# Kernel optimization log

Measured on AMD Instinct MI355X. Metric: run time of the kernel, lower is better.

The kernel has to match this reference:

```python
import jax, jax.numpy as jnp
import numpy as np

B, S, H, NH = 8, 512, 1024, 16
HD = H // NH          # 64
MAXP = 512            # max_position_embeddings


def setup_inputs() -> dict:
    key = jax.random.key(0)
    ks = jax.random.split(key, 6)
    sc = 0.02
    return {
        "hidden_states": jax.random.normal(ks[0], (B, S, H), jnp.float32),
        "attention_mask": jnp.zeros((B, 1, 1, S), jnp.float32),
        "Wq": jax.random.normal(ks[1], (H, H), jnp.float32) * sc,
        "bq": jnp.zeros((H,), jnp.float32),
        "Wk": jax.random.normal(ks[2], (H, H), jnp.float32) * sc,
        "bk": jnp.zeros((H,), jnp.float32),
        "Wv": jax.random.normal(ks[3], (H, H), jnp.float32) * sc,
        "bv": jnp.zeros((H,), jnp.float32),
        "dist_emb": jax.random.normal(ks[4], (2 * MAXP - 1, HD), jnp.float32) * sc,
    }


def reference(hidden_states, attention_mask, Wq, bq, Wk, bk, Wv, bv, dist_emb):
    b, s, h = hidden_states.shape
    nh, hd = NH, h // NH

    def heads(x):  # [b,s,h] -> [b,nh,s,hd]
        return x.reshape(b, s, nh, hd).transpose(0, 2, 1, 3)

    q = heads(hidden_states @ Wq.T + bq)
    k = heads(hidden_states @ Wk.T + bk)
    v = heads(hidden_states @ Wv.T + bv)

    # raw QK^T scores [b,nh,s,s]
    scores = jnp.einsum("bhld,bhrd->bhlr", q, k)

    # relative_key positional bias
    dist = jnp.arange(s)[:, None] - jnp.arange(s)[None, :] + (MAXP - 1)
    pos = dist_emb[dist]  # [s,s,hd]
    scores = scores + jnp.einsum("bhld,lrd->bhlr", q, pos)

    scores = scores / jnp.sqrt(jnp.asarray(hd, scores.dtype))
    scores = scores + attention_mask  # additive mask, broadcasts [b,1,1,s]

    probs = jax.nn.softmax(scores, axis=-1)  # dropout p=0 (eval)
    ctx = jnp.einsum("bhlr,bhrd->bhld", probs, v)
    ctx = ctx.transpose(0, 2, 1, 3).reshape(b, s, h)
    return ctx
```

## Files before the change

kernel.cpp:

```cpp
#include <hip/hip_runtime.h>

#define BB 8
#define SS 512
#define HH 1024
#define NHH 16
#define HDD 64

typedef short short8 __attribute__((ext_vector_type(8)));
typedef float f32x4 __attribute__((ext_vector_type(4)));
typedef unsigned short ushort;

union U4S8 { unsigned u[4]; short8 s; uint4 v; };

__device__ __forceinline__ void split2(float f0, float f1,
                                       unsigned& hi, unsigned& lo)
{
    unsigned u0 = __builtin_bit_cast(unsigned, f0);
    unsigned u1 = __builtin_bit_cast(unsigned, f1);
    hi = __builtin_amdgcn_perm(u1, u0, 0x07060302u);
    float r0 = f0 - __builtin_bit_cast(float, u0 & 0xffff0000u);
    float r1 = f1 - __builtin_bit_cast(float, u1 & 0xffff0000u);
    unsigned v0 = __builtin_bit_cast(unsigned, r0);
    unsigned v1 = __builtin_bit_cast(unsigned, r1);
    lo = __builtin_amdgcn_perm(v1, v0, 0x07060302u);
}

__device__ __forceinline__ unsigned pack_hi2(float f0, float f1) {
    return __builtin_amdgcn_perm(__builtin_bit_cast(unsigned, f1),
                                 __builtin_bit_cast(unsigned, f0), 0x07060302u);
}
__device__ __forceinline__ ushort bf16_rne(float f) {
    unsigned u = __builtin_bit_cast(unsigned, f);
    u += 0x7fffu + ((u >> 16) & 1u);
    return (ushort)(u >> 16);
}
__device__ __forceinline__ ushort bf16_tr(float f) {
    return (ushort)(__builtin_bit_cast(unsigned, f) >> 16);
}
__device__ __forceinline__ float bf16f(ushort s) {
    unsigned u = ((unsigned)s) << 16;
    return __builtin_bit_cast(float, u);
}
__device__ __forceinline__ int swel(int row, int col) {
    return row * 64 + ((((col >> 3) ^ (row & 7)) << 3) | (col & 7));
}

__global__ __launch_bounds__(256)
void qkv_proj_kernel(const float* __restrict__ HS,
                     const float* __restrict__ Wq, const float* __restrict__ bq,
                     const float* __restrict__ Wk, const float* __restrict__ bk,
                     const float* __restrict__ Wv, const float* __restrict__ bv,
                     ushort* __restrict__ Qh, ushort* __restrict__ Ql,
                     ushort* __restrict__ Kh, ushort* __restrict__ Kl,
                     ushort* __restrict__ Vh, ushort* __restrict__ Vl)
{
    const int bx = blockIdx.x;
    const int by = blockIdx.y;
    const int z   = bx >> 3;
    const int nf0 = (bx & 7) * 128;
    const int m0  = by * 128;

    const float* W    = (z == 0) ? Wq : (z == 1) ? Wk : Wv;
    const float* bias = (z == 0) ? bq : (z == 1) ? bk : bv;
    ushort* OutH = (z == 0) ? Qh : (z == 1) ? Kh : Vh;
    ushort* OutL = (z == 0) ? Ql : (z == 1) ? Kl : Vl;
    const float sc = (z == 0) ? 0.125f : 1.0f;

    __shared__ short Ah[128][32];
    __shared__ short Al[128][32];
    __shared__ short Bh[128][32];
    __shared__ short Bl[128][32];

    const int tid  = threadIdx.x;
    const int lane = tid & 63;
    const int wave = tid >> 6;
    const int wm   = (wave & 1) * 64;
    const int wn   = (wave >> 1) * 64;

    const int srow = tid >> 1;
    const int skh  = (tid & 1) * 16;

    const int fr    = lane & 15;
    const int kslot = lane >> 4;

    f32x4 acc[4][4];
#pragma unroll
    for (int i = 0; i < 4; i++)
#pragma unroll
        for (int j = 0; j < 4; j++) acc[i][j] = (f32x4)0.0f;

    for (int k0 = 0; k0 < HH; k0 += 32) {
        __syncthreads();
        {
            float ra[16], rb[16];
            const float* pa = HS + (size_t)(m0 + srow) * HH + k0 + skh;
            const float* pb = W + (size_t)(nf0 + srow) * HH + k0 + skh;
#pragma unroll
            for (int u = 0; u < 4; u++) {
                *(float4*)&ra[4 * u] = *(const float4*)(pa + 4 * u);
                *(float4*)&rb[4 * u] = *(const float4*)(pb + 4 * u);
            }
            unsigned ha[8], la[8], hb[8], lb[8];
#pragma unroll
            for (int p = 0; p < 8; p++) {
                split2(ra[2 * p], ra[2 * p + 1], ha[p], la[p]);
                split2(rb[2 * p], rb[2 * p + 1], hb[p], lb[p]);
            }
            *(uint4*)&Ah[srow][skh]     = *(uint4*)&ha[0];
            *(uint4*)&Ah[srow][skh + 8] = *(uint4*)&ha[4];
            *(uint4*)&Al[srow][skh]     = *(uint4*)&la[0];
            *(uint4*)&Al[srow][skh + 8] = *(uint4*)&la[4];
            *(uint4*)&Bh[srow][skh]     = *(uint4*)&hb[0];
            *(uint4*)&Bh[srow][skh + 8] = *(uint4*)&hb[4];
            *(uint4*)&Bl[srow][skh]     = *(uint4*)&lb[0];
            *(uint4*)&Bl[srow][skh + 8] = *(uint4*)&lb[4];
        }
        __syncthreads();

        short8 a_h[4], a_l[4], b_h[4], b_l[4];
#pragma unroll
        for (int i = 0; i < 4; i++) {
            a_h[i] = *(const short8*)&Ah[wm + i * 16 + fr][kslot * 8];
            a_l[i] = *(const short8*)&Al[wm + i * 16 + fr][kslot * 8];
            b_h[i] = *(const short8*)&Bh[wn + i * 16 + fr][kslot * 8];
            b_l[i] = *(const short8*)&Bl[wn + i * 16 + fr][kslot * 8];
        }
#pragma unroll
        for (int i = 0; i < 4; i++)
#pragma unroll
            for (int j = 0; j < 4; j++) {
                acc[i][j] = __builtin_amdgcn_mfma_f32_16x16x32_bf16(a_h[i], b_h[j], acc[i][j], 0, 0, 0);
                acc[i][j] = __builtin_amdgcn_mfma_f32_16x16x32_bf16(a_h[i], b_l[j], acc[i][j], 0, 0, 0);
                acc[i][j] = __builtin_amdgcn_mfma_f32_16x16x32_bf16(a_l[i], b_h[j], acc[i][j], 0, 0, 0);
            }
    }

    const int cn  = lane & 15;
    const int rm4 = (lane >> 4) * 4;
#pragma unroll
    for (int j = 0; j < 4; j++) {
        const int nn = nf0 + wn + j * 16 + cn;
        const int h  = nn >> 6;
        const int hd = nn & 63;
        const float bval = bias[nn];
#pragma unroll
        for (int i = 0; i < 4; i++) {
            const int mmb = m0 + wm + i * 16 + rm4;
            const int bi  = mmb >> 9;
            const int s0  = mmb & 511;
            const size_t base = (((size_t)(bi * NHH + h) * SS + s0) * HDD + hd);
#pragma unroll
            for (int r = 0; r < 4; r++) {
                const float val = (acc[i][j][r] + bval) * sc;
                const ushort hb = bf16_tr(val);
                const ushort lb2 = bf16_tr(val - bf16f(hb));
                OutH[base + (size_t)r * HDD] = hb;
                OutL[base + (size_t)r * HDD] = lb2;
            }
        }
    }
}

__global__ __launch_bounds__(512, 4)
void attn_mfma2_kernel(const ushort* __restrict__ Qh, const ushort* __restrict__ Ql,
                       const ushort* __restrict__ Kh, const ushort* __restrict__ Kl,
                       const ushort* __restrict__ Vh, const ushort* __restrict__ Vl,
                       const float* __restrict__ mask, const float* __restrict__ demb,
                       float* __restrict__ out)
{
    const int qt = blockIdx.x, h = blockIdx.y, b = blockIdx.z;
    const int l0 = qt * 64;
    const int tid  = threadIdx.x;
    const int lane = tid & 63;
    const int wave = tid >> 6;
    const int wl = wave >> 2;
    const int wr = wave & 3;
    const int fr = lane & 15;
    const int q4 = lane >> 4;
    const int brow = wr * 16 + fr;

    __shared__ short Thf[3 * 64 * 68];
    __shared__ short KhS[4096], KlS[4096];
    __shared__ short VthS[4096], VtlS[4096];
    __shared__ short PhS[4096], PlS[4096];
    __shared__ float Ms[64];
    __shared__ float rowsumw[4][64];

    const size_t bh = (size_t)(b * NHH + h) * SS * HDD;
    const f32x4 fz = {0.f, 0.f, 0.f, 0.f};

    short8 qh[4], ql[4];
#pragma unroll
    for (int i = 0; i < 2; i++)
#pragma unroll
        for (int ks = 0; ks < 2; ks++) {
            const size_t off = bh + (size_t)(l0 + wl * 32 + i * 16 + fr) * HDD + ks * 32 + q4 * 8;
            qh[i * 2 + ks] = *(const short8*)(Qh + off);
            ql[i * 2 + ks] = *(const short8*)(Ql + off);
        }

    auto chunk = [&](int jt, int slot) {
        f32x4 tacc[2]; tacc[0] = fz; tacc[1] = fz;
#pragma unroll
        for (int ks = 0; ks < 2; ks++) {
            int jrow = l0 + jt * 64 + brow;
            if (jrow > 1022) jrow = 1022;
            const float* ds = demb + (size_t)jrow * HDD + ks * 32 + q4 * 8;
            float4 v0 = *(const float4*)ds;
            float4 v1 = *(const float4*)(ds + 4);
            U4S8 dh;
            dh.u[0] = pack_hi2(v0.x, v0.y); dh.u[1] = pack_hi2(v0.z, v0.w);
            dh.u[2] = pack_hi2(v1.x, v1.y); dh.u[3] = pack_hi2(v1.z, v1.w);
#pragma unroll
            for (int i = 0; i < 2; i++)
                tacc[i] = __builtin_amdgcn_mfma_f32_16x16x32_bf16(qh[i * 2 + ks], dh.s, tacc[i], 0, 0, 0);
        }
#pragma unroll
        for (int i = 0; i < 2; i++)
#pragma unroll
            for (int r = 0; r < 4; r++)
                Thf[slot * 4352 + (wl * 32 + i * 16 + q4 * 4 + r) * 68 + brow] = (short)bf16_rne(tacc[i][r]);
    };

    chunk(8, 2);
    chunk(7, 1);

    f32x4 ctx[2]; ctx[0] = fz; ctx[1] = fz;
    float rs[2][4] = {{0.f, 0.f, 0.f, 0.f}, {0.f, 0.f, 0.f, 0.f}};

    const int srow = tid >> 3;
    const int sd   = (tid & 7) * 8;
    const int sel  = srow * 64 + (((sd >> 3) ^ (srow & 7)) << 3);
    const int vrow = lane;
    const int vd   = wave * 8;

    for (int rt = 0; rt < 8; rt++) {
        const int r0 = rt * 64;
        __syncthreads();

        {
            const size_t off = bh + (size_t)(r0 + srow) * HDD + sd;
            *(uint4*)&KhS[sel] = *(const uint4*)(Kh + off);
            *(uint4*)&KlS[sel] = *(const uint4*)(Kl + off);
        }
        {
            const size_t off = bh + (size_t)(r0 + vrow) * HDD + vd;
            short8 vh8 = *(const short8*)(Vh + off);
            short8 vl8 = *(const short8*)(Vl + off);
#pragma unroll
            for (int u = 0; u < 8; u++) {
                const int el = swel(vd + u, vrow);
                VthS[el] = vh8[u];
                VtlS[el] = vl8[u];
            }
        }
        if (tid < 64) Ms[tid] = mask[(size_t)b * SS + r0 + tid];
        __syncthreads();

        f32x4 sacc[2]; sacc[0] = fz; sacc[1] = fz;
#pragma unroll
        for (int ks = 0; ks < 2; ks++) {
            const int bel = brow * 64 + ((((ks * 4) + q4) ^ (brow & 7)) << 3);
            short8 kh8 = *(const short8*)&KhS[bel];
            short8 kl8 = *(const short8*)&KlS[bel];
#pragma unroll
            for (int i = 0; i < 2; i++) {
                sacc[i] = __builtin_amdgcn_mfma_f32_16x16x32_bf16(qh[i * 2 + ks], kh8, sacc[i], 0, 0, 0);
                sacc[i] = __builtin_amdgcn_mfma_f32_16x16x32_bf16(qh[i * 2 + ks], kl8, sacc[i], 0, 0, 0);
                sacc[i] = __builtin_amdgcn_mfma_f32_16x16x32_bf16(ql[i * 2 + ks], kh8, sacc[i], 0, 0, 0);
            }
        }

#pragma unroll
        for (int i = 0; i < 2; i++)
#pragma unroll
            for (int r = 0; r < 4; r++) {
                const int li  = wl * 32 + i * 16 + q4 * 4 + r;
                const int jjg = li + 511 - (r0 + brow);
                const int jt2 = jjg >> 6;
                const int slot = jt2 - (jt2 >= 3 ? 3 : 0) - (jt2 >= 6 ? 3 : 0);
                const float tb = bf16f((ushort)Thf[slot * 4352 + li * 68 + (jjg & 63)]);
                const float logit = sacc[i][r] + tb + Ms[brow];
                const float p = __expf(logit);
                rs[i][r] += p;
                const ushort phb = bf16_tr(p);
                const float plo = p - bf16f(phb);
                const int el = swel(li, brow);
                PhS[el] = (short)phb;
                PlS[el] = (short)bf16_tr(plo);
            }
        __syncthreads();

#pragma unroll
        for (int ks = 0; ks < 2; ks++) {
            const int belv = brow * 64 + ((((ks * 4) + q4) ^ (brow & 7)) << 3);
            short8 vh8 = *(const short8*)&VthS[belv];
            short8 vl8 = *(const short8*)&VtlS[belv];
#pragma unroll
            for (int i = 0; i < 2; i++) {
                const int arow = wl * 32 + i * 16 + fr;
                const int ael = arow * 64 + ((((ks * 4) + q4) ^ (arow & 7)) << 3);
                short8 ph8 = *(const short8*)&PhS[ael];
                short8 pl8 = *(const short8*)&PlS[ael];
                ctx[i] = __builtin_amdgcn_mfma_f32_16x16x32_bf16(ph8, vh8, ctx[i], 0, 0, 0);
                ctx[i] = __builtin_amdgcn_mfma_f32_16x16x32_bf16(ph8, vl8, ctx[i], 0, 0, 0);
                ctx[i] = __builtin_amdgcn_mfma_f32_16x16x32_bf16(pl8, vh8, ctx[i], 0, 0, 0);
            }
        }

        if (rt < 7) {
            const int jt2 = 6 - rt;
            chunk(jt2, jt2 % 3);
        }
    }

    __syncthreads();
#pragma unroll
    for (int i = 0; i < 2; i++)
#pragma unroll
        for (int r = 0; r < 4; r++) {
            float v = rs[i][r];
            v += __shfl_xor(v, 1);
            v += __shfl_xor(v, 2);
            v += __shfl_xor(v, 4);
            v += __shfl_xor(v, 8);
            if (fr == 0) rowsumw[wr][wl * 32 + i * 16 + q4 * 4 + r] = v;
        }
    __syncthreads();

#pragma unroll
    for (int i = 0; i < 2; i++)
#pragma unroll
        for (int r = 0; r < 4; r++) {
            const int li = wl * 32 + i * 16 + q4 * 4 + r;
            const float s = rowsumw[0][li] + rowsumw[1][li] + rowsumw[2][li] + rowsumw[3][li];
            out[((size_t)(b * SS + l0 + li)) * HH + h * HDD + wr * 16 + fr] = ctx[i][r] / s;
        }
}

extern "C" void kernel_launch(void* const* d_in, const int* in_sizes, int n_in,
                              void* d_out, int out_size, void* d_ws, size_t ws_size,
                              hipStream_t stream)
{
    const float* HS   = (const float*)d_in[0];
    const float* mask = (const float*)d_in[1];
    const float* Wq   = (const float*)d_in[2];
    const float* bq   = (const float*)d_in[3];
    const float* Wk   = (const float*)d_in[4];
    const float* bk   = (const float*)d_in[5];
    const float* Wv   = (const float*)d_in[6];
    const float* bv   = (const float*)d_in[7];
    const float* demb = (const float*)d_in[8];
    float* out = (float*)d_out;

    const size_t per = (size_t)BB * NHH * SS * HDD;
    ushort* Qh = (ushort*)d_ws;
    ushort* Ql = Qh + per;
    ushort* Kh = Ql + per;
    ushort* Kl = Kh + per;
    ushort* Vh = Kl + per;
    ushort* Vl = Vh + per;

    dim3 gp(24, 32);
    qkv_proj_kernel<<<gp, 256, 0, stream>>>(HS, Wq, bq, Wk, bk, Wv, bv,
                                            Qh, Ql, Kh, Kl, Vh, Vl);

    dim3 ga(SS / 64, NHH, BB);
    attn_mfma2_kernel<<<ga, 512, 0, stream>>>(Qh, Ql, Kh, Kl, Vh, Vl, mask, demb, out);
}
```

Baseline: 290.9 us.

## Register-prefetch next K/V tile and reorder grid so heads share K/V in cache

Loads the next 64-row K and V tiles into registers while the current tile is processed, so global memory latency overlaps MFMA work instead of stalling before each LDS store. It also flattens the grid to 1D with batch-head as the fastest index, so blocks scheduled together belong to different heads rather than the same head. This raises register pressure under launch_bounds(512,4) and may reduce L2 reuse of K/V between query tiles of one head.

```diff
diff --git a/kernel.cpp b/kernel.cpp
--- a/kernel.cpp
+++ b/kernel.cpp
@@ -168,8 +168,12 @@
                        const float* __restrict__ mask, const float* __restrict__ demb,
                        float* __restrict__ out)
 {
-    const int qt = blockIdx.x, h = blockIdx.y, b = blockIdx.z;
-    const int l0 = qt * 64;
+    const int bid = blockIdx.x;
+    const int hb  = bid & 127;
+    const int qt  = bid >> 7;
+    const int h   = hb & 15;
+    const int b   = hb >> 4;
+    const int l0  = qt * 64;
     const int tid  = threadIdx.x;
     const int lane = tid & 63;
     const int wave = tid >> 6;
@@ -186,7 +190,7 @@
     __shared__ float Ms[64];
     __shared__ float rowsumw[4][64];
 
-    const size_t bh = (size_t)(b * NHH + h) * SS * HDD;
+    const size_t bh_off = (size_t)(b * NHH + h) * SS * HDD;
     const f32x4 fz = {0.f, 0.f, 0.f, 0.f};
 
     short8 qh[4], ql[4];
@@ -194,7 +198,7 @@
     for (int i = 0; i < 2; i++)
 #pragma unroll
         for (int ks = 0; ks < 2; ks++) {
-            const size_t off = bh + (size_t)(l0 + wl * 32 + i * 16 + fr) * HDD + ks * 32 + q4 * 8;
+            const size_t off = bh_off + (size_t)(l0 + wl * 32 + i * 16 + fr) * HDD + ks * 32 + q4 * 8;
             qh[i * 2 + ks] = *(const short8*)(Qh + off);
             ql[i * 2 + ks] = *(const short8*)(Ql + off);
         }
@@ -234,27 +238,39 @@
     const int vrow = lane;
     const int vd   = wave * 8;
 
+    short8 kh_cur, kl_cur, vh_cur, vl_cur;
+    {
+        const size_t offK = bh_off + (size_t)srow * HDD + sd;
+        const size_t offV = bh_off + (size_t)vrow * HDD + vd;
+        kh_cur = *(const short8*)(Kh + offK);
+        kl_cur = *(const short8*)(Kl + offK);
+        vh_cur = *(const short8*)(Vh + offV);
+        vl_cur = *(const short8*)(Vl + offV);
+    }
+    short8 kh_nxt = kh_cur, kl_nxt = kl_cur, vh_nxt = vh_cur, vl_nxt = vl_cur;
+
     for (int rt = 0; rt < 8; rt++) {
         const int r0 = rt * 64;
         __syncthreads();
 
-        {
-            const size_t off = bh + (size_t)(r0 + srow) * HDD + sd;
-            *(uint4*)&KhS[sel] = *(const uint4*)(Kh + off);
-            *(uint4*)&KlS[sel] = *(const uint4*)(Kl + off);
-        }
-        {
-            const size_t off = bh + (size_t)(r0 + vrow) * HDD + vd;
-            short8 vh8 = *(const short8*)(Vh + off);
-            short8 vl8 = *(const short8*)(Vl + off);
-#pragma unroll
-            for (int u = 0; u < 8; u++) {
-                const int el = swel(vd + u, vrow);
-                VthS[el] = vh8[u];
-                VtlS[el] = vl8[u];
-            }
+        *(short8*)&KhS[sel] = kh_cur;
+        *(short8*)&KlS[sel] = kl_cur;
+#pragma unroll
+        for (int u = 0; u < 8; u++) {
+            const int el = swel(vd + u, vrow);
+            VthS[el] = vh_cur[u];
+            VtlS[el] = vl_cur[u];
         }
         if (tid < 64) Ms[tid] = mask[(size_t)b * SS + r0 + tid];
+
+        if (rt < 7) {
+            const size_t offK = bh_off + (size_t)(r0 + 64 + srow) * HDD + sd;
+            const size_t offV = bh_off + (size_t)(r0 + 64 + vrow) * HDD + vd;
+            kh_nxt = *(const short8*)(Kh + offK);
+            kl_nxt = *(const short8*)(Kl + offK);
+            vh_nxt = *(const short8*)(Vh + offV);
+            vl_nxt = *(const short8*)(Vl + offV);
+        }
         __syncthreads();
 
         f32x4 sacc[2]; sacc[0] = fz; sacc[1] = fz;
@@ -312,6 +328,9 @@
             const int jt2 = 6 - rt;
             chunk(jt2, jt2 % 3);
         }
+
+        kh_cur = kh_nxt; kl_cur = kl_nxt;
+        vh_cur = vh_nxt; vl_cur = vl_nxt;
     }
 
     __syncthreads();
@@ -365,6 +384,6 @@
     qkv_proj_kernel<<<gp, 256, 0, stream>>>(HS, Wq, bq, Wk, bk, Wv, bv,
                                             Qh, Ql, Kh, Kl, Vh, Vl);
 
-    dim3 ga(SS / 64, NHH, BB);
-    attn_mfma2_kernel<<<ga, 512, 0, stream>>>(Qh, Ql, Kh, Kl, Vh, Vl, mask, demb, out);
-}
+    attn_mfma2_kernel<<<dim3(BB * NHH * (SS / 64)), 512, 0, stream>>>(
+        Qh, Ql, Kh, Kl, Vh, Vl, mask, demb, out);
+}
```

Result: slower. 321.3 us (+10.5%).

## Pre-split fp32 inputs to bf16 hi/lo and stage GEMM tiles via direct global-to-LDS loads

Applied to the files above, without the earlier changes.

Adds a separate pass that converts the hidden states and the three weight matrices once into bf16 high/low halves in workspace. The projection GEMM then loads these bf16 tiles straight into LDS with global_load_lds, dropping the per-tile fp32 loads and split arithmetic from the main loop. Before this, each weight element was re-split for every M tile and each hidden-state element for every N tile. The cost is an extra kernel launch, an extra read and write of the converted data, and a larger workspace.

```diff
diff --git a/kernel.cpp b/kernel.cpp
--- a/kernel.cpp
+++ b/kernel.cpp
@@ -44,32 +44,71 @@
 __device__ __forceinline__ int swel(int row, int col) {
     return row * 64 + ((((col >> 3) ^ (row & 7)) << 3) | (col & 7));
 }
+__device__ __forceinline__ void gload16(const ushort* g, ushort* lds) {
+    __builtin_amdgcn_global_load_lds(
+        (const __attribute__((address_space(1))) unsigned int*)g,
+        (__attribute__((address_space(3))) unsigned int*)lds, 16, 0, 0);
+}
 
 __global__ __launch_bounds__(256)
-void qkv_proj_kernel(const float* __restrict__ HS,
-                     const float* __restrict__ Wq, const float* __restrict__ bq,
-                     const float* __restrict__ Wk, const float* __restrict__ bk,
-                     const float* __restrict__ Wv, const float* __restrict__ bv,
-                     ushort* __restrict__ Qh, ushort* __restrict__ Ql,
-                     ushort* __restrict__ Kh, ushort* __restrict__ Kl,
-                     ushort* __restrict__ Vh, ushort* __restrict__ Vl)
+void presplit_kernel(const float* __restrict__ HS, const float* __restrict__ Wq,
+                     const float* __restrict__ Wk, const float* __restrict__ Wv,
+                     ushort* __restrict__ Hh, ushort* __restrict__ Hl,
+                     ushort* __restrict__ Wh, ushort* __restrict__ Wl)
+{
+    const int HS4 = (BB * SS * HH) / 4;
+    const int W4  = (HH * HH) / 4;
+    const int tot = HS4 + 3 * W4;
+    for (int i = blockIdx.x * blockDim.x + threadIdx.x; i < tot;
+         i += gridDim.x * blockDim.x) {
+        float4 v;
+        ushort* dh; ushort* dl; size_t o4;
+        if (i < HS4) {
+            v = ((const float4*)HS)[i];
+            dh = Hh; dl = Hl; o4 = (size_t)i * 4;
+        } else {
+            const int j = i - HS4;
+            const int z = j / W4;
+            const int r = j - z * W4;
+            const float* W = (z == 0) ? Wq : (z == 1) ? Wk : Wv;
+            v = ((const float4*)W)[r];
+            dh = Wh; dl = Wl; o4 = (size_t)z * HH * HH + (size_t)r * 4;
+        }
+        unsigned h0, l0, h1, l1;
+        split2(v.x, v.y, h0, l0);
+        split2(v.z, v.w, h1, l1);
+        uint2 hv; hv.x = h0; hv.y = h1;
+        uint2 lv; lv.x = l0; lv.y = l1;
+        *(uint2*)(dh + o4) = hv;
+        *(uint2*)(dl + o4) = lv;
+    }
+}
+
+__global__ __launch_bounds__(256)
+void qkv_proj2_kernel(const ushort* __restrict__ Hh, const ushort* __restrict__ Hl,
+                      const ushort* __restrict__ Wh, const ushort* __restrict__ Wl,
+                      const float* __restrict__ bq, const float* __restrict__ bk,
+                      const float* __restrict__ bv,
+                      ushort* __restrict__ Qh, ushort* __restrict__ Ql,
+                      ushort* __restrict__ Kh, ushort* __restrict__ Kl,
+                      ushort* __restrict__ Vh, ushort* __restrict__ Vl)
 {
     const int bx = blockIdx.x;
     const int by = blockIdx.y;
     const int z   = bx >> 3;
     const int nf0 = (bx & 7) * 128;
     const int m0  = by * 128;
-
-    const float* W    = (z == 0) ? Wq : (z == 1) ? Wk : Wv;
+    const size_t wz = (size_t)z * HH * HH;
+
     const float* bias = (z == 0) ? bq : (z == 1) ? bk : bv;
     ushort* OutH = (z == 0) ? Qh : (z == 1) ? Kh : Vh;
     ushort* OutL = (z == 0) ? Ql : (z == 1) ? Kl : Vl;
     const float sc = (z == 0) ? 0.125f : 1.0f;
 
-    __shared__ short Ah[128][32];
-    __shared__ short Al[128][32];
-    __shared__ short Bh[128][32];
-    __shared__ short Bl[128][32];
+    __shared__ ushort AhS[128 * 32];
+    __shared__ ushort AlS[128 * 32];
+    __shared__ ushort BhS[128 * 32];
+    __shared__ ushort BlS[128 * 32];
 
     const int tid  = threadIdx.x;
     const int lane = tid & 63;
@@ -77,8 +116,8 @@
     const int wm   = (wave & 1) * 64;
     const int wn   = (wave >> 1) * 64;
 
-    const int srow = tid >> 1;
-    const int skh  = (tid & 1) * 16;
+    const int lrow = lane >> 2;
+    const int lch  = (lane & 3) * 8;
 
     const int fr    = lane & 15;
     const int kslot = lane >> 4;
@@ -91,39 +130,25 @@
 
     for (int k0 = 0; k0 < HH; k0 += 32) {
         __syncthreads();
-        {
-            float ra[16], rb[16];
-            const float* pa = HS + (size_t)(m0 + srow) * HH + k0 + skh;
-            const float* pb = W + (size_t)(nf0 + srow) * HH + k0 + skh;
-#pragma unroll
-            for (int u = 0; u < 4; u++) {
-                *(float4*)&ra[4 * u] = *(const float4*)(pa + 4 * u);
-                *(float4*)&rb[4 * u] = *(const float4*)(pb + 4 * u);
-            }
-            unsigned ha[8], la[8], hb[8], lb[8];
-#pragma unroll
-            for (int p = 0; p < 8; p++) {
-                split2(ra[2 * p], ra[2 * p + 1], ha[p], la[p]);
-                split2(rb[2 * p], rb[2 * p + 1], hb[p], lb[p]);
-            }
-            *(uint4*)&Ah[srow][skh]     = *(uint4*)&ha[0];
-            *(uint4*)&Ah[srow][skh + 8] = *(uint4*)&ha[4];
-            *(uint4*)&Al[srow][skh]     = *(uint4*)&la[0];
-            *(uint4*)&Al[srow][skh + 8] = *(uint4*)&la[4];
-            *(uint4*)&Bh[srow][skh]     = *(uint4*)&hb[0];
-            *(uint4*)&Bh[srow][skh + 8] = *(uint4*)&hb[4];
-            *(uint4*)&Bl[srow][skh]     = *(uint4*)&lb[0];
-            *(uint4*)&Bl[srow][skh + 8] = *(uint4*)&lb[4];
+#pragma unroll
+        for (int c = 0; c < 2; c++) {
+            const int r = wave * 32 + c * 16;
+            const size_t ga = (size_t)(m0 + r + lrow) * HH + k0 + lch;
+            const size_t gb = wz + (size_t)(nf0 + r + lrow) * HH + k0 + lch;
+            gload16(Hh + ga, &AhS[r * 32]);
+            gload16(Hl + ga, &AlS[r * 32]);
+            gload16(Wh + gb, &BhS[r * 32]);
+            gload16(Wl + gb, &BlS[r * 32]);
         }
         __syncthreads();
 
         short8 a_h[4], a_l[4], b_h[4], b_l[4];
 #pragma unroll
         for (int i = 0; i < 4; i++) {
-            a_h[i] = *(const short8*)&Ah[wm + i * 16 + fr][kslot * 8];
-            a_l[i] = *(const short8*)&Al[wm + i * 16 + fr][kslot * 8];
-            b_h[i] = *(const short8*)&Bh[wn + i * 16 + fr][kslot * 8];
-            b_l[i] = *(const short8*)&Bl[wn + i * 16 + fr][kslot * 8];
+            a_h[i] = *(const short8*)&AhS[(wm + i * 16 + fr) * 32 + kslot * 8];
+            a_l[i] = *(const short8*)&AlS[(wm + i * 16 + fr) * 32 + kslot * 8];
+            b_h[i] = *(const short8*)&BhS[(wn + i * 16 + fr) * 32 + kslot * 8];
+            b_l[i] = *(const short8*)&BlS[(wn + i * 16 + fr) * 32 + kslot * 8];
         }
 #pragma unroll
         for (int i = 0; i < 4; i++)
@@ -354,16 +379,23 @@
     float* out = (float*)d_out;
 
     const size_t per = (size_t)BB * NHH * SS * HDD;
+    const size_t wper = (size_t)3 * HH * HH;
     ushort* Qh = (ushort*)d_ws;
     ushort* Ql = Qh + per;
     ushort* Kh = Ql + per;
     ushort* Kl = Kh + per;
     ushort* Vh = Kl + per;
     ushort* Vl = Vh + per;
+    ushort* Hh = Vl + per;
+    ushort* Hl = Hh + per;
+    ushort* Wh = Hl + per;
+    ushort* Wl = Wh + wper;
+
+    presplit_kernel<<<2048, 256, 0, stream>>>(HS, Wq, Wk, Wv, Hh, Hl, Wh, Wl);
 
     dim3 gp(24, 32);
-    qkv_proj_kernel<<<gp, 256, 0, stream>>>(HS, Wq, bq, Wk, bk, Wv, bv,
-                                            Qh, Ql, Kh, Kl, Vh, Vl);
+    qkv_proj2_kernel<<<gp, 256, 0, stream>>>(Hh, Hl, Wh, Wl, bq, bk, bv,
+                                             Qh, Ql, Kh, Kl, Vh, Vl);
 
     dim3 ga(SS / 64, NHH, BB);
     attn_mfma2_kernel<<<ga, 512, 0, stream>>>(Qh, Ql, Kh, Kl, Vh, Vl, mask, demb, out);
```

After: 309.0 us. 6.2% more time.
